# Performance work log

Hardware: AMD Instinct MI355X
Metric: run time of the kernel (lower is better)

The kernel has to match this reference:

```python
import jax, jax.numpy as jnp
import numpy as np

N_EMBD = 1024
N_HEAD = 16
HEAD_DIM = N_EMBD // N_HEAD
B, T = 8, 1024


def setup_inputs() -> dict:
    key = jax.random.key(0)
    k1, k2, k3, k4 = jax.random.split(key, 4)
    x = jax.random.normal(k1, (B, T, N_EMBD), dtype=jnp.float32)
    # nn.Linear weight shapes: qkv (3C, C) no bias; proj (C, C) with bias
    w_qkv = jax.random.normal(k2, (3 * N_EMBD, N_EMBD), dtype=jnp.float32) * 0.02
    w_proj = jax.random.normal(k3, (N_EMBD, N_EMBD), dtype=jnp.float32) * 0.02
    b_proj = jax.random.normal(k4, (N_EMBD,), dtype=jnp.float32) * 0.02
    return {"x": x, "w_qkv": w_qkv, "w_proj": w_proj, "b_proj": b_proj}


def reference(x, w_qkv, w_proj, b_proj):
    Bq, Tq, C = x.shape
    qkv = jnp.einsum('btc,dc->btd', x, w_qkv)  # (B,T,3C)
    q, k, v = jnp.split(qkv, 3, axis=-1)
    def heads(t):
        return t.reshape(Bq, Tq, N_HEAD, HEAD_DIM).transpose(0, 2, 1, 3)  # (B,H,T,D)
    q, k, v = heads(q), heads(k), heads(v)
    scale = 1.0 / np.sqrt(HEAD_DIM).astype(np.float32)
    att = jnp.einsum('bhqd,bhkd->bhqk', q, k) * scale  # (B,H,T,T)
    causal = jnp.tril(jnp.ones((Tq, Tq), dtype=bool))
    att = jnp.where(causal, att, -jnp.inf)
    att = jax.nn.softmax(att, axis=-1)
    # dropout: eval mode -> identity
    y = jnp.einsum('bhqk,bhkd->bhqd', att, v)
    y = y.transpose(0, 2, 1, 3).reshape(Bq, Tq, C)
    return jnp.einsum('btc,dc->btd', y, w_proj) + b_proj
```

## Files before the change

kernel.cpp:

```cpp
#include <hip/hip_runtime.h>
#include <stdint.h>


#define Bn 8
#define Tn 1024
#define Cn 1024
#define Hn 16
#define Dn 64
#define Mn (Bn * Tn)
#define NQKV (3 * Cn)
#define QKS 2048

typedef unsigned short u16;
typedef float f32x4 __attribute__((ext_vector_type(4)));
typedef __bf16 bf16x8 __attribute__((ext_vector_type(8)));
typedef unsigned short ushx8 __attribute__((ext_vector_type(8)));
typedef unsigned short ushx4 __attribute__((ext_vector_type(4)));

__device__ __forceinline__ u16 f2bf(float f) {
  unsigned int u = __float_as_uint(f);
  u += 0x7fffu + ((u >> 16) & 1u);
  return (u16)(u >> 16);
}
__device__ __forceinline__ u16 f2bf_rna(float f) {
  return (u16)((__float_as_uint(f) + 0x8000u) >> 16);
}

__device__ __forceinline__ f32x4 mfma_bf16(ushx8 a, ushx8 b, f32x4 c) {
  return __builtin_amdgcn_mfma_f32_16x16x32_bf16(
      __builtin_bit_cast(bf16x8, a), __builtin_bit_cast(bf16x8, b), c, 0, 0, 0);
}

__device__ __forceinline__ void async16(const u16* g, u16* l) {
  __builtin_amdgcn_global_load_lds(
      (__attribute__((address_space(1))) void*)(void*)g,
      (__attribute__((address_space(3))) void*)l, 16, 0, 0);
}

template <int CTRL>
__device__ __forceinline__ float dppmov(float v) {
  return __builtin_bit_cast(float, __builtin_amdgcn_update_dpp(
      0, __builtin_bit_cast(int, v), CTRL, 0xf, 0xf, true));
}
__device__ __forceinline__ float red16max(float v) {
  v = fmaxf(v, dppmov<0xB1>(v));
  v = fmaxf(v, dppmov<0x4E>(v));
  v = fmaxf(v, dppmov<0x141>(v));
  v = fmaxf(v, dppmov<0x140>(v));
  return v;
}
__device__ __forceinline__ float red16sum(float v) {
  v += dppmov<0xB1>(v);
  v += dppmov<0x4E>(v);
  v += dppmov<0x141>(v);
  v += dppmov<0x140>(v);
  return v;
}

__global__ void cast3_kernel(const float* __restrict__ a, u16* __restrict__ oa, int na4,
                             const float* __restrict__ b, u16* __restrict__ ob, int nb4,
                             const float* __restrict__ c, u16* __restrict__ oc, int nc4) {
  int i = blockIdx.x * blockDim.x + threadIdx.x;
  const float* in;
  u16* out;
  if (i < na4) { in = a; out = oa; }
  else if (i < na4 + nb4) { in = b; out = ob; i -= na4; }
  else if (i < na4 + nb4 + nc4) { in = c; out = oc; i -= na4 + nb4; }
  else return;
  float4 v = ((const float4*)in)[i];
  ushx4 o = { f2bf(v.x), f2bf(v.y), f2bf(v.z), f2bf(v.w) };
  ((ushx4*)out)[i] = o;
}

#define SLOG2E 0.18033688011112042f

template <int MODE>
__device__ __forceinline__ void gemm_body(
    const u16* __restrict__ A, const u16* __restrict__ Bw,
    void* __restrict__ Cout, u16* __restrict__ vt,
    const float* __restrict__ bias) {
  __shared__ alignas(16) u16 lds[36864];

  const int tid = threadIdx.x;
  const int lane = tid & 63;
  const int wv = tid >> 6;
  const int quad = lane >> 4;
  const int l16 = lane & 15;
  const int wr = wv >> 1;
  const int wc = wv & 1;

  const int xcd = blockIdx.x & 7;
  const int loc = blockIdx.x >> 3;
  const int m0 = (xcd * 4 + (loc & 3)) * 256;
  const int n0 = (loc >> 2) * 128;

  const u16* gA = A + (size_t)m0 * Cn;
  const u16* gB = Bw + (size_t)n0 * Cn;

  const int r0s = tid >> 2;
  const int q0s = (tid & 3) ^ ((r0s >> 1) & 3);
  const int c1s = 512 + tid;
  const int r1s = c1s >> 2;
  const int q1s = (c1s & 3) ^ ((r1s >> 1) & 3);
  const int so0 = r0s * Cn + q0s * 8;
  const int so1 = r1s * Cn + q1s * 8;

  auto stageA = [&](int slot, int h) {
    u16* dst = lds + slot * 8192 + tid * 8;
    const u16* src = gA + (h >> 1) * 64 + (h & 1) * 32;
    async16(src + so0, dst);
    async16(src + so1, dst + 4096);
  };
  auto stageB = [&](int slot, int h) {
    u16* dst = lds + 24576 + slot * 4096 + tid * 8;
    const u16* src = gB + (h >> 1) * 64 + (h & 1) * 32;
    async16(src + so0, dst);
  };

  const int sread = (quad ^ ((l16 >> 1) & 3)) * 8;
  const int aoff = (wr * 64 + l16) * 32 + sread;
  const int boff = 24576 + (wc * 64 + l16) * 32 + sread;

  f32x4 acc[4][4];
#pragma unroll
  for (int i = 0; i < 4; ++i)
#pragma unroll
    for (int jj = 0; jj < 4; ++jj) acc[i][jj] = (f32x4){0.f, 0.f, 0.f, 0.f};
  ushx8 af[4], bfr[4];

  stageA(0, 0); stageB(0, 0);
  stageA(1, 1); stageB(1, 1);
  asm volatile("s_waitcnt vmcnt(3)" ::: "memory");
  __builtin_amdgcn_s_barrier();
  asm volatile("" ::: "memory");

#define PH(slot, sslot, hd)                                                    \
  {                                                                            \
    const u16* ab_ = lds + (slot) * 8192 + aoff;                               \
    af[0] = *(const ushx8*)(ab_);                                              \
    af[1] = *(const ushx8*)(ab_ + 512);                                        \
    af[2] = *(const ushx8*)(ab_ + 1024);                                       \
    af[3] = *(const ushx8*)(ab_ + 1536);                                       \
    const u16* bb_ = lds + (slot) * 4096 + boff;                               \
    bfr[0] = *(const ushx8*)(bb_);                                             \
    bfr[1] = *(const ushx8*)(bb_ + 512);                                       \
    bfr[2] = *(const ushx8*)(bb_ + 1024);                                      \
    bfr[3] = *(const ushx8*)(bb_ + 1536);                                      \
    stageA((sslot), (hd));                                                     \
    stageB((sslot), (hd));                                                     \
    asm volatile("" ::: "memory");                                             \
    __builtin_amdgcn_s_barrier();                                              \
    asm volatile("s_waitcnt lgkmcnt(0)" ::: "memory");                         \
    __builtin_amdgcn_s_setprio(1);                                             \
    _Pragma("unroll") for (int mi_ = 0; mi_ < 4; ++mi_) {                      \
      _Pragma("unroll") for (int ni_ = 0; ni_ < 4; ++ni_) {                    \
        acc[mi_][ni_] = mfma_bf16(af[mi_], bfr[ni_], acc[mi_][ni_]);           \
      }                                                                        \
    }                                                                          \
    __builtin_amdgcn_s_setprio(0);                                             \
    asm volatile("s_waitcnt vmcnt(3)" ::: "memory");                           \
    asm volatile("" ::: "memory");                                             \
    __builtin_amdgcn_s_barrier();                                              \
    asm volatile("" ::: "memory");                                             \
  }

#pragma unroll 1
  for (int it = 0; it < 5; ++it) {
    const int p = it * 6;
    PH(0, 2, p + 2)
    PH(1, 0, p + 3)
    PH(2, 1, p + 4)
    PH(0, 2, p + 5)
    PH(1, 0, p + 6)
    PH(2, 1, p + 7)
  }
  PH(0, 2, 31)
  PH(1, 0, 31)
#undef PH
  asm volatile("s_waitcnt vmcnt(0)" ::: "memory");

  if constexpr (MODE) {
    if (n0 < 2 * Cn) {
      const float sc = (n0 < Cn) ? SLOG2E : 1.f;
#pragma unroll
      for (int mi = 0; mi < 4; ++mi) {
#pragma unroll
        for (int ni = 0; ni < 4; ++ni) {
          const int col = n0 + wc * 64 + ni * 16 + l16;
          const int row = m0 + wr * 64 + mi * 16 + quad * 4;
#pragma unroll
          for (int i = 0; i < 4; ++i)
            ((u16*)Cout)[(size_t)(row + i) * QKS + col] = f2bf(acc[mi][ni][i] * sc);
        }
      }
    } else {
#pragma unroll
      for (int mi = 0; mi < 4; ++mi) {
#pragma unroll
        for (int ni = 0; ni < 4; ++ni) {
          const int colV = n0 - 2 * Cn + wc * 64 + ni * 16 + l16;
          const int hh = colV >> 6, dd = colV & 63;
          const int row0 = m0 + wr * 64 + mi * 16 + quad * 4;
          const int bb = row0 >> 10, tt = row0 & 1023;
          unsigned int lo = (unsigned int)f2bf(acc[mi][ni][0]) |
                            ((unsigned int)f2bf(acc[mi][ni][1]) << 16);
          unsigned int hi = (unsigned int)f2bf(acc[mi][ni][2]) |
                            ((unsigned int)f2bf(acc[mi][ni][3]) << 16);
          uint2 pk = {lo, hi};
          *(uint2*)&vt[((size_t)(bb * Hn + hh) * Dn + dd) * Tn + tt] = pk;
        }
      }
    }
  } else {
#pragma unroll
    for (int mi = 0; mi < 4; ++mi) {
#pragma unroll
      for (int ni = 0; ni < 4; ++ni) {
        const int col = n0 + wc * 64 + ni * 16 + l16;
        const float bv = bias[col];
        const int row = m0 + wr * 64 + mi * 16 + quad * 4;
#pragma unroll
        for (int i = 0; i < 4; ++i)
          ((float*)Cout)[(size_t)(row + i) * Cn + col] = acc[mi][ni][i] + bv;
      }
    }
  }
}

template <int BM, int MODE>
__device__ __forceinline__ void gemm_body4(
    const u16* __restrict__ A, const u16* __restrict__ Bw,
    void* __restrict__ Cout, u16* __restrict__ vt,
    const float* __restrict__ bias) {
  constexpr int ASLOT = BM * 32;
  constexpr int BSLOT = 128 * 32;
  constexpr int BBASE = 3 * ASLOT;
  constexpr int ASW = BM / 64;
  constexpr int BSW = 2;
  constexpr int LOADS = ASW + BSW;
  constexpr int MREP = BM / 32;
  constexpr int MT = Mn / BM;
  constexpr int MPX = MT / 8;

  __shared__ alignas(16) u16 lds[3 * (ASLOT + BSLOT)];

  const int tid = threadIdx.x;
  const int lane = tid & 63;
  const int wv = tid >> 6;
  const int quad = lane >> 4;
  const int l16 = lane & 15;
  const int wr = wv >> 1;
  const int wc = wv & 1;

  const int xcd = blockIdx.x & 7;
  const int loc = blockIdx.x >> 3;
  const int m0 = (xcd * MPX + (loc & (MPX - 1))) * BM;
  const int n0 = (loc / MPX) * 128;

  const u16* gA = A + (size_t)m0 * Cn;
  const u16* gB = Bw + (size_t)n0 * Cn;

  int soff[4];
#pragma unroll
  for (int s = 0; s < 4; ++s) {
    int c = s * 256 + tid;
    int row = c >> 2;
    int q = (c & 3) ^ ((row >> 1) & 3);
    soff[s] = row * Cn + q * 8;
  }

  auto stage = [&](int slot, int h) {
    const u16* sA = gA + (h >> 1) * 64 + (h & 1) * 32;
    u16* dA = lds + slot * ASLOT + tid * 8;
#pragma unroll
    for (int s = 0; s < ASW; ++s) async16(sA + soff[s], dA + s * 2048);
    const u16* sB = gB + (h >> 1) * 64 + (h & 1) * 32;
    u16* dB = lds + BBASE + slot * BSLOT + tid * 8;
#pragma unroll
    for (int s = 0; s < BSW; ++s) async16(sB + soff[s], dB + s * 2048);
  };

  const int sread = (quad ^ ((l16 >> 1) & 3)) * 8;
  const int aoff = (wr * (BM / 2) + l16) * 32 + sread;
  const int boff = BBASE + (wc * 64 + l16) * 32 + sread;

  f32x4 acc[MREP][4];
#pragma unroll
  for (int i = 0; i < MREP; ++i)
#pragma unroll
    for (int jj = 0; jj < 4; ++jj) acc[i][jj] = (f32x4){0.f, 0.f, 0.f, 0.f};
  ushx8 af[MREP], bfr[4];

  stage(0, 0);
  stage(1, 1);
  if constexpr (LOADS == 6) asm volatile("s_waitcnt vmcnt(6)" ::: "memory");
  else asm volatile("s_waitcnt vmcnt(4)" ::: "memory");
  __builtin_amdgcn_s_barrier();
  asm volatile("" ::: "memory");

#define PH(slot, sslot, hd)                                                    \
  {                                                                            \
    const u16* ab_ = lds + (slot) * ASLOT + aoff;                              \
    _Pragma("unroll") for (int mi_ = 0; mi_ < MREP; ++mi_)                     \
      af[mi_] = *(const ushx8*)(ab_ + mi_ * 512);                              \
    const u16* bb_ = lds + (slot) * BSLOT + boff;                              \
    _Pragma("unroll") for (int ni_ = 0; ni_ < 4; ++ni_)                        \
      bfr[ni_] = *(const ushx8*)(bb_ + ni_ * 512);                             \
    stage((sslot), (hd));                                                      \
    asm volatile("" ::: "memory");                                             \
    __builtin_amdgcn_s_barrier();                                              \
    asm volatile("s_waitcnt lgkmcnt(0)" ::: "memory");                         \
    __builtin_amdgcn_s_setprio(1);                                             \
    _Pragma("unroll") for (int mi_ = 0; mi_ < MREP; ++mi_) {                   \
      _Pragma("unroll") for (int ni_ = 0; ni_ < 4; ++ni_) {                    \
        acc[mi_][ni_] = mfma_bf16(af[mi_], bfr[ni_], acc[mi_][ni_]);           \
      }                                                                        \
    }                                                                          \
    __builtin_amdgcn_s_setprio(0);                                             \
    if constexpr (LOADS == 6)                                                  \
      asm volatile("s_waitcnt vmcnt(6)" ::: "memory");                         \
    else                                                                       \
      asm volatile("s_waitcnt vmcnt(4)" ::: "memory");                         \
    asm volatile("" ::: "memory");                                             \
    __builtin_amdgcn_s_barrier();                                              \
    asm volatile("" ::: "memory");                                             \
  }

#pragma unroll 1
  for (int it = 0; it < 5; ++it) {
    const int p = it * 6;
    PH(0, 2, p + 2)
    PH(1, 0, p + 3)
    PH(2, 1, p + 4)
    PH(0, 2, p + 5)
    PH(1, 0, p + 6)
    PH(2, 1, p + 7)
  }
  PH(0, 2, 31)
  PH(1, 0, 31)
#undef PH
  asm volatile("s_waitcnt vmcnt(0)" ::: "memory");

  if constexpr (MODE) {
  } else {
#pragma unroll
    for (int mi = 0; mi < MREP; ++mi) {
#pragma unroll
      for (int ni = 0; ni < 4; ++ni) {
        const int col = n0 + wc * 64 + ni * 16 + l16;
        const float bv = bias[col];
        const int row = m0 + wr * (BM / 2) + mi * 16 + quad * 4;
#pragma unroll
        for (int i = 0; i < 4; ++i)
          ((float*)Cout)[(size_t)(row + i) * Cn + col] = acc[mi][ni][i] + bv;
      }
    }
  }
}

__global__ __launch_bounds__(512, 4) void gemm_qkv_k(
    const u16* __restrict__ A, const u16* __restrict__ Bw,
    u16* __restrict__ qk, u16* __restrict__ vt) {
  gemm_body<1>(A, Bw, (void*)qk, vt, nullptr);
}
__global__ __launch_bounds__(256, 2) void gemm_proj_k(
    const u16* __restrict__ A, const u16* __restrict__ Bw,
    float* __restrict__ out, const float* __restrict__ bias) {
  gemm_body4<128, 0>(A, Bw, (void*)out, nullptr, bias);
}

__global__ __launch_bounds__(512, 4) void attn_kernel(
    const u16* __restrict__ qk, const u16* __restrict__ vt,
    u16* __restrict__ out) {
  const int j = blockIdx.x, h = blockIdx.y, b = blockIdx.z;
  const int tid = threadIdx.x;
  const int lane = tid & 63;
  const int wv = tid >> 6;
  const int quad = lane >> 4;
  const int l16 = lane & 15;

  __shared__ alignas(16) u16 Ks[3][64 * 64];
  __shared__ alignas(16) u16 Vts[3][64 * 64];
  __shared__ alignas(16) u16 Ps[8][16 * 72];

  const u16* qb = qk + (size_t)b * Tn * QKS + h * Dn;
  const u16* kb = qk + (size_t)b * Tn * QKS + Cn + h * Dn;
  const u16* vtb = vt + (size_t)(b * Hn + h) * Dn * Tn;

  const int srow = tid >> 3;
  const int sgc = (tid & 7) ^ (srow & 7);
  u16* pswv = Ps[wv];

  auto stageKV = [&](int slot, int kt) {
    const int kv0s = kt * 64;
    async16(kb + (size_t)(kv0s + srow) * QKS + sgc * 8, Ks[slot] + tid * 8);
    async16(vtb + (size_t)srow * Tn + kv0s + sgc * 8, Vts[slot] + tid * 8);
  };

#pragma unroll 1
  for (int ph = 0; ph < 2; ++ph) {
    const int qt = ph ? (7 - j) : j;
    const int q0w = qt * 128 + wv * 16;
    const int ntiles = 2 * qt + 2;
    const int tdiag = q0w >> 6;

    ushx8 qf[2];
    {
      const u16* qp = qb + (size_t)(q0w + l16) * QKS + quad * 8;
      qf[0] = *(const ushx8*)qp;
      qf[1] = *(const ushx8*)(qp + 32);
    }

    f32x4 o[4];
#pragma unroll
    for (int nt = 0; nt < 4; ++nt) o[nt] = (f32x4){0.f, 0.f, 0.f, 0.f};
    float mrow[4], lrow[4];
#pragma unroll
    for (int i = 0; i < 4; ++i) { mrow[i] = -__builtin_inff(); lrow[i] = 0.f; }

    auto qkt = [&](f32x4* s, const u16* ks) {
#pragma unroll
      for (int nt = 0; nt < 4; ++nt) s[nt] = (f32x4){0.f, 0.f, 0.f, 0.f};
#pragma unroll
      for (int nt = 0; nt < 4; ++nt) {
        const int rb = nt * 16 + l16;
        ushx8 b0 = *(const ushx8*)(ks + rb * 64 + (quad ^ (rb & 7)) * 8);
        ushx8 b1 = *(const ushx8*)(ks + rb * 64 + ((quad + 4) ^ (rb & 7)) * 8);
        s[nt] = mfma_bf16(qf[0], b0, s[nt]);
        s[nt] = mfma_bf16(qf[1], b1, s[nt]);
      }
    };

    auto smpv = [&](f32x4* s, int tt, const u16* vs) {
      const int kv0 = tt * 64;
      if (tt == tdiag) {
#pragma unroll
        for (int i = 0; i < 4; ++i) {
          const int qr = q0w + quad * 4 + i;
          float vv[4];
          float rmax = -__builtin_inff();
#pragma unroll
          for (int nt = 0; nt < 4; ++nt) {
            float v = s[nt][i];
            if ((kv0 + nt * 16 + l16) > qr) v = -__builtin_inff();
            vv[nt] = v;
            rmax = fmaxf(rmax, v);
          }
          rmax = red16max(rmax);
          const float mnew = fmaxf(mrow[i], rmax);
          const float al = __builtin_amdgcn_exp2f(mrow[i] - mnew);
          mrow[i] = mnew;
          float rsum = 0.f;
#pragma unroll
          for (int nt = 0; nt < 4; ++nt) {
            float p = __builtin_amdgcn_exp2f(vv[nt] - mnew);
            rsum += p;
            pswv[(quad * 4 + i) * 72 + nt * 16 + l16] = f2bf_rna(p);
          }
          lrow[i] = lrow[i] * al + rsum;
#pragma unroll
          for (int nt = 0; nt < 4; ++nt) o[nt][i] *= al;
        }
      } else {
#pragma unroll
        for (int i = 0; i < 4; ++i) {
          float rmax = fmaxf(fmaxf(s[0][i], s[1][i]), fmaxf(s[2][i], s[3][i]));
          rmax = red16max(rmax);
          const float mnew = fmaxf(mrow[i], rmax);
          const float al = __builtin_amdgcn_exp2f(mrow[i] - mnew);
          mrow[i] = mnew;
          float rsum = 0.f;
#pragma unroll
          for (int nt = 0; nt < 4; ++nt) {
            float p = __builtin_amdgcn_exp2f(s[nt][i] - mnew);
            rsum += p;
            pswv[(quad * 4 + i) * 72 + nt * 16 + l16] = f2bf_rna(p);
          }
          lrow[i] = lrow[i] * al + rsum;
#pragma unroll
          for (int nt = 0; nt < 4; ++nt) o[nt][i] *= al;
        }
      }
      ushx8 pf0, pf1;
      {
        const u16* pp = pswv + l16 * 72 + quad * 8;
        pf0 = *(const ushx8*)pp;
        pf1 = *(const ushx8*)(pp + 32);
      }
#pragma unroll
      for (int nt = 0; nt < 4; ++nt) {
        const int rb = nt * 16 + l16;
        ushx8 v0 = *(const ushx8*)(vs + rb * 64 + (quad ^ (rb & 7)) * 8);
        ushx8 v1 = *(const ushx8*)(vs + rb * 64 + ((quad + 4) ^ (rb & 7)) * 8);
        o[nt] = mfma_bf16(pf0, v0, o[nt]);
        o[nt] = mfma_bf16(pf1, v1, o[nt]);
      }
    };

    __syncthreads();
    stageKV(0, 0);
    stageKV(1, 1);

#pragma unroll 1
    for (int t = 0; t < ntiles; t += 2) {
      const int s0 = t % 3;
      const int s1 = (t + 1) % 3;
      __syncthreads();

      if (t + 2 < ntiles) stageKV((t + 2) % 3, t + 2);

      const bool a1 = (t <= tdiag);
      const bool a2 = (t + 1 <= tdiag);

      f32x4 sA[4], sB[4];
      if (a1) qkt(sA, Ks[s0]);
      if (a2) qkt(sB, Ks[s1]);
      if (a1) smpv(sA, t, Vts[s0]);

      __syncthreads();
      if (t + 3 < ntiles) stageKV((t + 3) % 3, t + 3);

      if (a2) smpv(sB, t + 1, Vts[s1]);
    }

#pragma unroll
    for (int i = 0; i < 4; ++i) {
      const float inv = 1.f / red16sum(lrow[i]);
      const int trow = q0w + quad * 4 + i;
      u16* op = out + ((size_t)(b * Tn + trow)) * Cn + h * Dn + l16;
#pragma unroll
      for (int nt = 0; nt < 4; ++nt) op[nt * 16] = f2bf(o[nt][i] * inv);
    }
  }
}

extern "C" void kernel_launch(void* const* d_in, const int* in_sizes, int n_in,
                              void* d_out, int out_size, void* d_ws, size_t ws_size,
                              hipStream_t stream) {
  const float* x = (const float*)d_in[0];
  const float* w_qkv = (const float*)d_in[1];
  const float* w_proj = (const float*)d_in[2];
  const float* b_proj = (const float*)d_in[3];
  float* out = (float*)d_out;
  char* ws = (char*)d_ws;

  u16* xb     = (u16*)(ws);
  u16* wqkvb  = (u16*)(ws + 16777216);
  u16* wprojb = (u16*)(ws + 23068672);
  u16* qkb    = (u16*)(ws + 25165824);
  u16* vtb    = (u16*)(ws + 58720256);
  u16* yb     = (u16*)(ws + 75497472);

  cast3_kernel<<<12288, 256, 0, stream>>>(x, xb, 2097152,
                                          w_qkv, wqkvb, 786432,
                                          w_proj, wprojb, 262144);

  gemm_qkv_k<<<768, 512, 0, stream>>>(xb, wqkvb, qkb, vtb);

  attn_kernel<<<dim3(4, Hn, Bn), 512, 0, stream>>>(qkb, vtb, yb);

  gemm_proj_k<<<512, 256, 0, stream>>>(yb, wprojb, out, b_proj);
}
```

Baseline: 214.1 us.

## Load QKV weight fragments directly from global in pre-tiled layout, bypassing LDS

```diff
diff --git a/kernel.cpp b/kernel.cpp
--- a/kernel.cpp
+++ b/kernel.cpp
@@ -61,25 +61,33 @@
                              const float* __restrict__ b, u16* __restrict__ ob, int nb4,
                              const float* __restrict__ c, u16* __restrict__ oc, int nc4) {
   int i = blockIdx.x * blockDim.x + threadIdx.x;
-  const float* in;
-  u16* out;
-  if (i < na4) { in = a; out = oa; }
-  else if (i < na4 + nb4) { in = b; out = ob; i -= na4; }
-  else if (i < na4 + nb4 + nc4) { in = c; out = oc; i -= na4 + nb4; }
-  else return;
-  float4 v = ((const float4*)in)[i];
-  ushx4 o = { f2bf(v.x), f2bf(v.y), f2bf(v.z), f2bf(v.w) };
-  ((ushx4*)out)[i] = o;
+  if (i < na4) {
+    float4 v = ((const float4*)a)[i];
+    ushx4 o = { f2bf(v.x), f2bf(v.y), f2bf(v.z), f2bf(v.w) };
+    ((ushx4*)oa)[i] = o;
+  } else if (i < na4 + nb4) {
+    i -= na4;
+    float4 v = ((const float4*)b)[i];
+    ushx4 o = { f2bf(v.x), f2bf(v.y), f2bf(v.z), f2bf(v.w) };
+    const int n = i >> 8;
+    const int k4 = i & 255;
+    const int kb = k4 >> 3;
+    const int kin = (k4 & 7) * 4;
+    *(ushx4*)&ob[((size_t)kb * NQKV + n) * 32 + kin] = o;
+  } else if (i < na4 + nb4 + nc4) {
+    i -= na4 + nb4;
+    float4 v = ((const float4*)c)[i];
+    ushx4 o = { f2bf(v.x), f2bf(v.y), f2bf(v.z), f2bf(v.w) };
+    ((ushx4*)oc)[i] = o;
+  }
 }
 
 #define SLOG2E 0.18033688011112042f
 
-template <int MODE>
-__device__ __forceinline__ void gemm_body(
+__global__ __launch_bounds__(512, 4) void gemm_qkv_k(
     const u16* __restrict__ A, const u16* __restrict__ Bw,
-    void* __restrict__ Cout, u16* __restrict__ vt,
-    const float* __restrict__ bias) {
-  __shared__ alignas(16) u16 lds[36864];
+    u16* __restrict__ qk, u16* __restrict__ vt) {
+  __shared__ alignas(16) u16 lds[24576];
 
   const int tid = threadIdx.x;
   const int lane = tid & 63;
@@ -95,7 +103,6 @@
   const int n0 = (loc >> 2) * 128;
 
   const u16* gA = A + (size_t)m0 * Cn;
-  const u16* gB = Bw + (size_t)n0 * Cn;
 
   const int r0s = tid >> 2;
   const int q0s = (tid & 3) ^ ((r0s >> 1) & 3);
@@ -111,54 +118,59 @@
     async16(src + so0, dst);
     async16(src + so1, dst + 4096);
   };
-  auto stageB = [&](int slot, int h) {
-    u16* dst = lds + 24576 + slot * 4096 + tid * 8;
-    const u16* src = gB + (h >> 1) * 64 + (h & 1) * 32;
-    async16(src + so0, dst);
-  };
+
+  const size_t bq0 = (size_t)(n0 + wc * 64 + l16) * 32 + quad * 8;
+  const u16* bbase = Bw + bq0;
 
   const int sread = (quad ^ ((l16 >> 1) & 3)) * 8;
   const int aoff = (wr * 64 + l16) * 32 + sread;
-  const int boff = 24576 + (wc * 64 + l16) * 32 + sread;
 
   f32x4 acc[4][4];
 #pragma unroll
   for (int i = 0; i < 4; ++i)
 #pragma unroll
     for (int jj = 0; jj < 4; ++jj) acc[i][jj] = (f32x4){0.f, 0.f, 0.f, 0.f};
-  ushx8 af[4], bfr[4];
-
-  stageA(0, 0); stageB(0, 0);
-  stageA(1, 1); stageB(1, 1);
-  asm volatile("s_waitcnt vmcnt(3)" ::: "memory");
+  ushx8 af[4], bcur[4], bnxt[4];
+
+  stageA(0, 0);
+#pragma unroll
+  for (int ni = 0; ni < 4; ++ni)
+    bcur[ni] = *(const ushx8*)(bbase + ni * 512);
+  stageA(1, 1);
+  asm volatile("s_waitcnt vmcnt(6)" ::: "memory");
   __builtin_amdgcn_s_barrier();
   asm volatile("" ::: "memory");
 
-#define PH(slot, sslot, hd)                                                    \
+#define PH(slot, sslot, p, BC, BN)                                             \
   {                                                                            \
     const u16* ab_ = lds + (slot) * 8192 + aoff;                               \
     af[0] = *(const ushx8*)(ab_);                                              \
     af[1] = *(const ushx8*)(ab_ + 512);                                        \
     af[2] = *(const ushx8*)(ab_ + 1024);                                       \
     af[3] = *(const ushx8*)(ab_ + 1536);                                       \
-    const u16* bb_ = lds + (slot) * 4096 + boff;                               \
-    bfr[0] = *(const ushx8*)(bb_);                                             \
-    bfr[1] = *(const ushx8*)(bb_ + 512);                                       \
-    bfr[2] = *(const ushx8*)(bb_ + 1024);                                      \
-    bfr[3] = *(const ushx8*)(bb_ + 1536);                                      \
-    stageA((sslot), (hd));                                                     \
-    stageB((sslot), (hd));                                                     \
+    {                                                                          \
+      const int kb_ = ((p) + 1 < 32) ? (p) + 1 : 31;                           \
+      const u16* bp_ = bbase + (size_t)kb_ * (NQKV * 32);                      \
+      BN[0] = *(const ushx8*)(bp_);                                            \
+      BN[1] = *(const ushx8*)(bp_ + 512);                                      \
+      BN[2] = *(const ushx8*)(bp_ + 1024);                                     \
+      BN[3] = *(const ushx8*)(bp_ + 1536);                                     \
+    }                                                                          \
+    {                                                                          \
+      const int hd_ = ((p) + 2 < 32) ? (p) + 2 : 31;                           \
+      stageA((sslot), hd_);                                                    \
+    }                                                                          \
     asm volatile("" ::: "memory");                                             \
     __builtin_amdgcn_s_barrier();                                              \
     asm volatile("s_waitcnt lgkmcnt(0)" ::: "memory");                         \
     __builtin_amdgcn_s_setprio(1);                                             \
     _Pragma("unroll") for (int mi_ = 0; mi_ < 4; ++mi_) {                      \
       _Pragma("unroll") for (int ni_ = 0; ni_ < 4; ++ni_) {                    \
-        acc[mi_][ni_] = mfma_bf16(af[mi_], bfr[ni_], acc[mi_][ni_]);           \
+        acc[mi_][ni_] = mfma_bf16(af[mi_], BC[ni_], acc[mi_][ni_]);            \
       }                                                                        \
     }                                                                          \
     __builtin_amdgcn_s_setprio(0);                                             \
-    asm volatile("s_waitcnt vmcnt(3)" ::: "memory");                           \
+    asm volatile("s_waitcnt vmcnt(6)" ::: "memory");                           \
     asm volatile("" ::: "memory");                                             \
     __builtin_amdgcn_s_barrier();                                              \
     asm volatile("" ::: "memory");                                             \
@@ -167,48 +179,29 @@
 #pragma unroll 1
   for (int it = 0; it < 5; ++it) {
     const int p = it * 6;
-    PH(0, 2, p + 2)
-    PH(1, 0, p + 3)
-    PH(2, 1, p + 4)
-    PH(0, 2, p + 5)
-    PH(1, 0, p + 6)
-    PH(2, 1, p + 7)
-  }
-  PH(0, 2, 31)
-  PH(1, 0, 31)
+    PH(0, 2, p + 0, bcur, bnxt)
+    PH(1, 0, p + 1, bnxt, bcur)
+    PH(2, 1, p + 2, bcur, bnxt)
+    PH(0, 2, p + 3, bnxt, bcur)
+    PH(1, 0, p + 4, bcur, bnxt)
+    PH(2, 1, p + 5, bnxt, bcur)
+  }
+  PH(0, 2, 30, bcur, bnxt)
+  PH(1, 0, 31, bnxt, bcur)
 #undef PH
   asm volatile("s_waitcnt vmcnt(0)" ::: "memory");
 
-  if constexpr (MODE) {
-    if (n0 < 2 * Cn) {
-      const float sc = (n0 < Cn) ? SLOG2E : 1.f;
-#pragma unroll
-      for (int mi = 0; mi < 4; ++mi) {
-#pragma unroll
-        for (int ni = 0; ni < 4; ++ni) {
-          const int col = n0 + wc * 64 + ni * 16 + l16;
-          const int row = m0 + wr * 64 + mi * 16 + quad * 4;
-#pragma unroll
-          for (int i = 0; i < 4; ++i)
-            ((u16*)Cout)[(size_t)(row + i) * QKS + col] = f2bf(acc[mi][ni][i] * sc);
-        }
-      }
-    } else {
-#pragma unroll
-      for (int mi = 0; mi < 4; ++mi) {
-#pragma unroll
-        for (int ni = 0; ni < 4; ++ni) {
-          const int colV = n0 - 2 * Cn + wc * 64 + ni * 16 + l16;
-          const int hh = colV >> 6, dd = colV & 63;
-          const int row0 = m0 + wr * 64 + mi * 16 + quad * 4;
-          const int bb = row0 >> 10, tt = row0 & 1023;
-          unsigned int lo = (unsigned int)f2bf(acc[mi][ni][0]) |
-                            ((unsigned int)f2bf(acc[mi][ni][1]) << 16);
-          unsigned int hi = (unsigned int)f2bf(acc[mi][ni][2]) |
-                            ((unsigned int)f2bf(acc[mi][ni][3]) << 16);
-          uint2 pk = {lo, hi};
-          *(uint2*)&vt[((size_t)(bb * Hn + hh) * Dn + dd) * Tn + tt] = pk;
-        }
+  if (n0 < 2 * Cn) {
+    const float sc = (n0 < Cn) ? SLOG2E : 1.f;
+#pragma unroll
+    for (int mi = 0; mi < 4; ++mi) {
+#pragma unroll
+      for (int ni = 0; ni < 4; ++ni) {
+        const int col = n0 + wc * 64 + ni * 16 + l16;
+        const int row = m0 + wr * 64 + mi * 16 + quad * 4;
+#pragma unroll
+        for (int i = 0; i < 4; ++i)
+          qk[(size_t)(row + i) * QKS + col] = f2bf(acc[mi][ni][i] * sc);
       }
     }
   } else {
@@ -216,22 +209,25 @@
     for (int mi = 0; mi < 4; ++mi) {
 #pragma unroll
       for (int ni = 0; ni < 4; ++ni) {
-        const int col = n0 + wc * 64 + ni * 16 + l16;
-        const float bv = bias[col];
-        const int row = m0 + wr * 64 + mi * 16 + quad * 4;
-#pragma unroll
-        for (int i = 0; i < 4; ++i)
-          ((float*)Cout)[(size_t)(row + i) * Cn + col] = acc[mi][ni][i] + bv;
+        const int colV = n0 - 2 * Cn + wc * 64 + ni * 16 + l16;
+        const int hh = colV >> 6, dd = colV & 63;
+        const int row0 = m0 + wr * 64 + mi * 16 + quad * 4;
+        const int bb = row0 >> 10, tt = row0 & 1023;
+        unsigned int lo = (unsigned int)f2bf(acc[mi][ni][0]) |
+                          ((unsigned int)f2bf(acc[mi][ni][1]) << 16);
+        unsigned int hi = (unsigned int)f2bf(acc[mi][ni][2]) |
+                          ((unsigned int)f2bf(acc[mi][ni][3]) << 16);
+        uint2 pk = {lo, hi};
+        *(uint2*)&vt[((size_t)(bb * Hn + hh) * Dn + dd) * Tn + tt] = pk;
       }
     }
   }
 }
 
-template <int BM, int MODE>
+template <int BM>
 __device__ __forceinline__ void gemm_body4(
     const u16* __restrict__ A, const u16* __restrict__ Bw,
-    void* __restrict__ Cout, u16* __restrict__ vt,
-    const float* __restrict__ bias) {
+    float* __restrict__ Cout, const float* __restrict__ bias) {
   constexpr int ASLOT = BM * 32;
   constexpr int BSLOT = 128 * 32;
   constexpr int BBASE = 3 * ASLOT;
@@ -341,32 +337,24 @@
 #undef PH
   asm volatile("s_waitcnt vmcnt(0)" ::: "memory");
 
-  if constexpr (MODE) {
-  } else {
-#pragma unroll
-    for (int mi = 0; mi < MREP; ++mi) {
-#pragma unroll
-      for (int ni = 0; ni < 4; ++ni) {
-        const int col = n0 + wc * 64 + ni * 16 + l16;
-        const float bv = bias[col];
-        const int row = m0 + wr * (BM / 2) + mi * 16 + quad * 4;
-#pragma unroll
-        for (int i = 0; i < 4; ++i)
-          ((float*)Cout)[(size_t)(row + i) * Cn + col] = acc[mi][ni][i] + bv;
-      }
+#pragma unroll
+  for (int mi = 0; mi < MREP; ++mi) {
+#pragma unroll
+    for (int ni = 0; ni < 4; ++ni) {
+      const int col = n0 + wc * 64 + ni * 16 + l16;
+      const float bv = bias[col];
+      const int row = m0 + wr * (BM / 2) + mi * 16 + quad * 4;
+#pragma unroll
+      for (int i = 0; i < 4; ++i)
+        Cout[(size_t)(row + i) * Cn + col] = acc[mi][ni][i] + bv;
     }
   }
 }
 
-__global__ __launch_bounds__(512, 4) void gemm_qkv_k(
-    const u16* __restrict__ A, const u16* __restrict__ Bw,
-    u16* __restrict__ qk, u16* __restrict__ vt) {
-  gemm_body<1>(A, Bw, (void*)qk, vt, nullptr);
-}
 __global__ __launch_bounds__(256, 2) void gemm_proj_k(
     const u16* __restrict__ A, const u16* __restrict__ Bw,
     float* __restrict__ out, const float* __restrict__ bias) {
-  gemm_body4<128, 0>(A, Bw, (void*)out, nullptr, bias);
+  gemm_body4<128>(A, Bw, out, bias);
 }
 
 __global__ __launch_bounds__(512, 4) void attn_kernel(
```

Measured after the change: 249.4 us. 1.16x slower.
